# Optimization experiments

Hardware: AMD Instinct MI355X
Metric: run time of the kernel (lower is better)

Reference implementation:

```python
import jax, jax.numpy as jnp
import numpy as np

N, E = 50000, 800000          # nodes, directed edges
IN_DIM, HC, OUT_DIM = 128, 64, 128
NEG_SLOPE = 0.2               # PyG GATConv default leaky_relu slope
EPS = 1e-5                    # PyG LayerNorm default eps


def setup_inputs() -> dict:
    key = jax.random.key(0)
    ks = jax.random.split(key, 10)
    s = 0.1
    return {
        "x": jax.random.normal(ks[0], (N, IN_DIM), jnp.float32),
        "edge_index": jax.random.randint(ks[1], (2, E), 0, N, dtype=jnp.int32),
        # conv1: GATConv(IN_DIM -> HC, heads=2, concat=True)
        "W1": jax.random.normal(ks[2], (IN_DIM, 2 * HC), jnp.float32) * s,
        "att_src1": jax.random.normal(ks[3], (2, HC), jnp.float32) * s,
        "att_dst1": jax.random.normal(ks[4], (2, HC), jnp.float32) * s,
        "b1": jnp.zeros((2 * HC,), jnp.float32),
        "ln1_w": jnp.ones((2 * HC,), jnp.float32),
        "ln1_b": jnp.zeros((2 * HC,), jnp.float32),
        # conv2: GATConv(2*HC -> OUT_DIM, heads=1, concat=False)
        "W2": jax.random.normal(ks[5], (2 * HC, OUT_DIM), jnp.float32) * s,
        "att_src2": jax.random.normal(ks[6], (1, OUT_DIM), jnp.float32) * s,
        "att_dst2": jax.random.normal(ks[7], (1, OUT_DIM), jnp.float32) * s,
        "b2": jnp.zeros((OUT_DIM,), jnp.float32),
        "ln2_w": jnp.ones((OUT_DIM,), jnp.float32),
        "ln2_b": jnp.zeros((OUT_DIM,), jnp.float32),
    }


def gat_conv(x, src, dst, W, att_src, att_dst, bias, heads, C, concat):
    """PyG GATConv (shared lin for src/dst, self-loops already in src/dst)."""
    n = x.shape[0]
    h = (x @ W).reshape(n, heads, C)                       # [N,H,C]
    a_src = jnp.einsum('nhc,hc->nh', h, att_src)           # [N,H]
    a_dst = jnp.einsum('nhc,hc->nh', h, att_dst)           # [N,H]
    e = jax.nn.leaky_relu(a_src[src] + a_dst[dst], NEG_SLOPE)   # [E',H]
    # numerically-stable softmax over incoming edges of each dst node
    emax = jax.ops.segment_max(e, dst, num_segments=n)     # [N,H] (self-loops => non-empty)
    ex = jnp.exp(e - emax[dst])
    denom = jax.ops.segment_sum(ex, dst, num_segments=n)
    alpha = ex / (denom[dst] + 1e-16)                      # [E',H]
    out = jax.ops.segment_sum(h[src] * alpha[:, :, None], dst, num_segments=n)  # [N,H,C]
    out = out.reshape(n, heads * C) if concat else out.mean(axis=1)
    return out + bias


def graph_layernorm(x, w, b):
    """PyG LayerNorm, mode='graph', single graph: normalize over ALL nodes+features."""
    mean = x.mean()
    xc = x - mean
    var = (xc * xc).mean()
    return xc * jax.lax.rsqrt(var + EPS) * w + b


def reference(x, edge_index, W1, att_src1, att_dst1, b1, ln1_w, ln1_b,
              W2, att_src2, att_dst2, b2, ln2_w, ln2_b):
    n = x.shape[0]
    loop = jnp.arange(n, dtype=edge_index.dtype)
    src = jnp.concatenate([edge_index[0], loop])           # add self-loops for GAT convs
    dst = jnp.concatenate([edge_index[1], loop])

    h = gat_conv(x, src, dst, W1, att_src1, att_dst1, b1, heads=2, C=HC, concat=True)
    h = jax.nn.relu(graph_layernorm(h, ln1_w, ln1_b))
    h = gat_conv(h, src, dst, W2, att_src2, att_dst2, b2, heads=1, C=OUT_DIM, concat=False)
    h = graph_layernorm(h, ln2_w, ln2_b)

    # SimpleConv(aggr='mean') over the ORIGINAL edges (no self-loops), then residual
    s0, d0 = edge_index[0], edge_index[1]
    agg = jax.ops.segment_sum(h[s0], d0, num_segments=n)
    cnt = jax.ops.segment_sum(jnp.ones(s0.shape, h.dtype), d0, num_segments=n)
    mean_agg = agg / jnp.maximum(cnt, 1.0)[:, None]
    return jax.nn.relu(mean_agg + x)
```

## Files before the change

kernel.cpp:

```cpp
#include <hip/hip_runtime.h>
#include <hip/hip_bf16.h>
#include <cstdint>
#include <cstddef>

#define NN 50000
#define EE 800000
#define DD 128
#define NEG 0.2f
#define EPSL 1e-5f

#define NB   196
#define EPB  4096
#define NBKT 196
#define HM   (NBKT * NB)

#define GROWS 64
#define AB    (NN / 8)

typedef __hip_bfloat16 bf16;
typedef short short8 __attribute__((ext_vector_type(8)));
typedef float f32x4 __attribute__((ext_vector_type(4)));

__device__ inline float bflo(unsigned u) { return __uint_as_float(u << 16); }
__device__ inline float bfhi(unsigned u) { return __uint_as_float(u & 0xffff0000u); }
__device__ inline float bf2f(unsigned short u) { return __uint_as_float((unsigned)u << 16); }

__device__ inline unsigned short f2bf(float f) {
    __bf16 h = (__bf16)f;
    return __builtin_bit_cast(unsigned short, h);
}
__device__ inline unsigned pack2(float a, float b) {
    return (unsigned)f2bf(a) | ((unsigned)f2bf(b) << 16);
}

__device__ inline void store4(float* Out, size_t idx, float4 v) {
    *(float4*)&Out[idx] = v;
}
__device__ inline void store4(bf16* Out, size_t idx, float4 v) {
    union { bf16 b[4]; ushort4 u; } cv;
    cv.b[0] = (bf16)v.x; cv.b[1] = (bf16)v.y; cv.b[2] = (bf16)v.z; cv.b[3] = (bf16)v.w;
    *(ushort4*)&Out[idx] = cv.u;
}


__global__ __launch_bounds__(256) void hist_kernel(const int* __restrict__ ei,
                                                   int* __restrict__ histG) {
    __shared__ int lh[NBKT];
    int tid = threadIdx.x;
    for (int t = tid; t < NBKT; t += 256) lh[t] = 0;
    __syncthreads();
    int base = blockIdx.x * EPB;
    #pragma unroll
    for (int j = 0; j < EPB / 1024; ++j) {
        int i4 = base + (j * 256 + tid) * 4;
        if (i4 < EE) {
            int4 d4 = *(const int4*)&ei[EE + i4];
            atomicAdd(&lh[(unsigned)d4.x >> 8], 1);
            atomicAdd(&lh[(unsigned)d4.y >> 8], 1);
            atomicAdd(&lh[(unsigned)d4.z >> 8], 1);
            atomicAdd(&lh[(unsigned)d4.w >> 8], 1);
        }
    }
    __syncthreads();
    for (int t = tid; t < NBKT; t += 256) histG[t * NB + blockIdx.x] = lh[t];
}

__global__ __launch_bounds__(1024) void scan_hist_kernel(const int* __restrict__ histG,
                                                         int* __restrict__ offs,
                                                         int* __restrict__ bstart) {
    __shared__ int wsum[16];
    __shared__ int carry_s;
    int tid = threadIdx.x, lane = tid & 63, wv = tid >> 6;
    if (tid == 0) carry_s = 0;
    __syncthreads();
    for (int base = 0; base < HM; base += 4096) {
        int i4 = base + tid * 4;
        int4 v = make_int4(0, 0, 0, 0);
        if (i4 + 3 < HM) v = *(const int4*)&histG[i4];
        else {
            if (i4 + 0 < HM) v.x = histG[i4 + 0];
            if (i4 + 1 < HM) v.y = histG[i4 + 1];
            if (i4 + 2 < HM) v.z = histG[i4 + 2];
            if (i4 + 3 < HM) v.w = histG[i4 + 3];
        }
        int tsum = v.x + v.y + v.z + v.w;
        int x = tsum;
        for (int off = 1; off < 64; off <<= 1) {
            int t = __shfl_up(x, off);
            if (lane >= off) x += t;
        }
        if (lane == 63) wsum[wv] = x;
        __syncthreads();
        if (wv == 0) {
            int s = (lane < 16) ? wsum[lane] : 0;
            for (int off = 1; off < 16; off <<= 1) {
                int t = __shfl_up(s, off);
                if (lane >= off) s += t;
            }
            if (lane < 16) wsum[lane] = s;
        }
        __syncthreads();
        int waveoff = (wv == 0) ? 0 : wsum[wv - 1];
        int carry = carry_s;
        int o0 = carry + waveoff + x - tsum;
        int o1 = o0 + v.x, o2 = o1 + v.y, o3 = o2 + v.z;
        if (i4 + 3 < HM) *(int4*)&offs[i4] = make_int4(o0, o1, o2, o3);
        else {
            if (i4 + 0 < HM) offs[i4 + 0] = o0;
            if (i4 + 1 < HM) offs[i4 + 1] = o1;
            if (i4 + 2 < HM) offs[i4 + 2] = o2;
            if (i4 + 3 < HM) offs[i4 + 3] = o3;
        }
        if (i4 < HM && (i4 % NB) == 0) bstart[i4 / NB] = o0;
        __syncthreads();
        if (tid == 0) carry_s += wsum[15];
        __syncthreads();
    }
    if (tid == 0) bstart[NBKT] = carry_s;
}

__global__ __launch_bounds__(256) void scatter_pass1_kernel(const int* __restrict__ ei,
                                                            const int* __restrict__ offs,
                                                            unsigned* __restrict__ tmp) {
    __shared__ int lofs[NBKT];
    int tid = threadIdx.x;
    for (int t = tid; t < NBKT; t += 256) lofs[t] = offs[t * NB + blockIdx.x];
    __syncthreads();
    int base = blockIdx.x * EPB;
    #pragma unroll
    for (int j = 0; j < EPB / 1024; ++j) {
        int i4 = base + (j * 256 + tid) * 4;
        if (i4 < EE) {
            int4 s4 = *(const int4*)&ei[i4];
            int4 d4 = *(const int4*)&ei[EE + i4];
            unsigned k0 = ((unsigned)d4.x << 16) | (unsigned)s4.x;
            unsigned k1 = ((unsigned)d4.y << 16) | (unsigned)s4.y;
            unsigned k2 = ((unsigned)d4.z << 16) | (unsigned)s4.z;
            unsigned k3 = ((unsigned)d4.w << 16) | (unsigned)s4.w;
            tmp[atomicAdd(&lofs[(unsigned)d4.x >> 8], 1)] = k0;
            tmp[atomicAdd(&lofs[(unsigned)d4.y >> 8], 1)] = k1;
            tmp[atomicAdd(&lofs[(unsigned)d4.z >> 8], 1)] = k2;
            tmp[atomicAdd(&lofs[(unsigned)d4.w >> 8], 1)] = k3;
        }
    }
}

__global__ __launch_bounds__(256) void bucket_sort_kernel(const unsigned* __restrict__ tmp,
                                                          const int* __restrict__ bstart,
                                                          unsigned* __restrict__ col,
                                                          int* __restrict__ row_ptr) {
    __shared__ int cnt[256];
    __shared__ int cpos[256];
    __shared__ int wtot[4];
    int tid = threadIdx.x, lane = tid & 63, wv = tid >> 6;
    int s0 = bstart[blockIdx.x], s1 = bstart[blockIdx.x + 1];
    cnt[tid] = 0;
    __syncthreads();
    for (int i = s0 + tid; i < s1; i += 256)
        atomicAdd(&cnt[(tmp[i] >> 16) & 0xFF], 1);
    __syncthreads();
    int v = cnt[tid];
    int x = v;
    for (int off = 1; off < 64; off <<= 1) {
        int t = __shfl_up(x, off);
        if (lane >= off) x += t;
    }
    if (lane == 63) wtot[wv] = x;
    __syncthreads();
    int add = 0;
    for (int k = 0; k < wv; ++k) add += wtot[k];
    int start = s0 + add + x - v;
    cpos[tid] = start;
    int d = blockIdx.x * 256 + tid;
    if (d <= NN) row_ptr[d] = start;
    __syncthreads();
    for (int i = s0 + tid; i < s1; i += 256) {
        unsigned key = tmp[i];
        int pos = atomicAdd(&cpos[(key >> 16) & 0xFF], 1);
        col[pos] = key;
    }
}

template <int H, bool LN, typename XT>
__global__ __launch_bounds__(512) void gemm_attn(const XT* __restrict__ X,
                                                 const float* __restrict__ W,
                                                 const float* __restrict__ att_s,
                                                 const float* __restrict__ att_d,
                                                 const double* __restrict__ stats,
                                                 const float* __restrict__ lnw,
                                                 const float* __restrict__ lnb,
                                                 bf16* __restrict__ Hout,
                                                 float* __restrict__ a_src,
                                                 float* __restrict__ a_dst) {
    __shared__ __align__(16) char lds[(128 * 136 + 64 * 136) * 2 + 2048];
    unsigned short* Bt = (unsigned short*)lds;
    unsigned short* As = (unsigned short*)(lds + 128 * 136 * 2);
    float* Cs = (float*)lds;
    float* psum = (float*)(lds + (128 * 136 + 64 * 136) * 2);

    int tid = threadIdx.x;
    int row0 = blockIdx.x * GROWS;

    {
        int c = tid & 127, kg = tid >> 7;
        #pragma unroll 2
        for (int i = 0; i < 8; ++i) {
            int k0 = i * 16 + kg * 4;
            float wa = W[(size_t)(k0 + 0) * DD + c];
            float wb = W[(size_t)(k0 + 1) * DD + c];
            float wcv = W[(size_t)(k0 + 2) * DD + c];
            float wdv = W[(size_t)(k0 + 3) * DD + c];
            uint2 pk = make_uint2(pack2(wa, wb), pack2(wcv, wdv));
            *(uint2*)&Bt[c * 136 + k0] = pk;
        }
    }
    {
        int sub = tid & 31, rq = tid >> 5;
        int c4 = sub * 4;
        float mean = 0.f, inv = 1.f;
        float4 lw4 = make_float4(1.f, 1.f, 1.f, 1.f), lb4 = make_float4(0.f, 0.f, 0.f, 0.f);
        if (LN) {
            const double M = (double)NN * DD;
            double mean_d = stats[0] / M;
            double var_d = stats[1] / M - mean_d * mean_d;
            mean = (float)mean_d;
            inv = rsqrtf((float)var_d + EPSL);
            lw4 = *(const float4*)&lnw[c4];
            lb4 = *(const float4*)&lnb[c4];
        }
        #pragma unroll
        for (int i = 0; i < 4; ++i) {
            int r = i * 16 + rq;
            int row = row0 + r;
            float4 xv = make_float4(0.f, 0.f, 0.f, 0.f);
            if (row < NN) {
                if constexpr (sizeof(XT) == 4) {
                    xv = *(const float4*)&((const float*)X)[(size_t)row * DD + c4];
                } else {
                    ushort4 xb = *(const ushort4*)&((const unsigned short*)X)[(size_t)row * DD + c4];
                    xv = make_float4(bf2f(xb.x), bf2f(xb.y), bf2f(xb.z), bf2f(xb.w));
                }
            }
            if (LN) {
                xv.x = fmaxf((xv.x - mean) * inv * lw4.x + lb4.x, 0.f);
                xv.y = fmaxf((xv.y - mean) * inv * lw4.y + lb4.y, 0.f);
                xv.z = fmaxf((xv.z - mean) * inv * lw4.z + lb4.z, 0.f);
                xv.w = fmaxf((xv.w - mean) * inv * lw4.w + lb4.w, 0.f);
            }
            uint2 pk = make_uint2(pack2(xv.x, xv.y), pack2(xv.z, xv.w));
            *(uint2*)&As[r * 136 + c4] = pk;
        }
    }
    __syncthreads();

    int lane = tid & 63, w = tid >> 6;
    int rg = w & 3, cg = w >> 2;
    int l15 = lane & 15, quad = lane >> 4;
    f32x4 acc[4];
    #pragma unroll
    for (int t = 0; t < 4; ++t) acc[t] = 0.f;
    const unsigned short* Arow = As + (rg * 16 + l15) * 136 + quad * 8;
    const unsigned short* Brow = Bt + l15 * 136 + quad * 8;
    #pragma unroll
    for (int ks = 0; ks < 4; ++ks) {
        short8 a = *(const short8*)(Arow + ks * 32);
        #pragma unroll
        for (int tt = 0; tt < 4; ++tt) {
            short8 b = *(const short8*)(Brow + (cg * 4 + tt) * 16 * 136 + ks * 32);
            acc[tt] = __builtin_amdgcn_mfma_f32_16x16x32_bf16(a, b, acc[tt], 0, 0, 0);
        }
    }
    __syncthreads();

    #pragma unroll
    for (int tt = 0; tt < 4; ++tt)
        #pragma unroll
        for (int r = 0; r < 4; ++r)
            Cs[(rg * 16 + quad * 4 + r) * 132 + (cg * 4 + tt) * 16 + l15] = acc[tt][r];

    float ds[4] = {0.f, 0.f, 0.f, 0.f}, dd[4] = {0.f, 0.f, 0.f, 0.f};
    #pragma unroll
    for (int tt = 0; tt < 4; ++tt) {
        int cc = (cg * 4 + tt) * 16 + l15;
        float as_ = att_s[cc], ad_ = att_d[cc];
        #pragma unroll
        for (int r = 0; r < 4; ++r) {
            ds[r] = fmaf(acc[tt][r], as_, ds[r]);
            dd[r] = fmaf(acc[tt][r], ad_, dd[r]);
        }
    }
    #pragma unroll
    for (int off = 1; off < 16; off <<= 1) {
        #pragma unroll
        for (int r = 0; r < 4; ++r) {
            ds[r] += __shfl_xor(ds[r], off);
            dd[r] += __shfl_xor(dd[r], off);
        }
    }
    if (l15 == 0) {
        #pragma unroll
        for (int r = 0; r < 4; ++r) {
            int rr = rg * 16 + quad * 4 + r;
            int row = row0 + rr;
            if (H == 2) {
                if (row < NN) {
                    a_src[row * 2 + cg] = ds[r];
                    a_dst[row * 2 + cg] = dd[r];
                }
            } else {
                psum[cg * 64 + rr] = ds[r];
                psum[128 + cg * 64 + rr] = dd[r];
            }
        }
    }
    __syncthreads();

    if (H == 1 && tid < 64) {
        int row = row0 + tid;
        if (row < NN) {
            a_src[row] = psum[tid] + psum[64 + tid];
            a_dst[row] = psum[128 + tid] + psum[192 + tid];
        }
    }

    {
        int sub = tid & 31, rq = tid >> 5;
        int c4 = sub * 4;
        unsigned short* Hp = (unsigned short*)Hout;
        #pragma unroll
        for (int i = 0; i < 4; ++i) {
            int r = i * 16 + rq;
            int row = row0 + r;
            if (row < NN) {
                float4 cv = *(const float4*)&Cs[r * 132 + c4];
                ushort4 pk;
                pk.x = f2bf(cv.x); pk.y = f2bf(cv.y);
                pk.z = f2bf(cv.z); pk.w = f2bf(cv.w);
                *(ushort4*)&Hp[(size_t)row * DD + c4] = pk;
            }
        }
    }
}

template <int H, typename OT>
__global__ __launch_bounds__(256) void gat_agg(const int* __restrict__ row_ptr,
                                               const unsigned* __restrict__ col,
                                               const bf16* __restrict__ Hin,
                                               const float* __restrict__ a_src,
                                               const float* __restrict__ a_dst,
                                               const float* __restrict__ bias,
                                               OT* __restrict__ Out,
                                               float2* __restrict__ pstats) {
    int tid = threadIdx.x;
    int sl = tid & 31;
    int hw = tid >> 5;
    int n = blockIdx.x * 8 + hw;
    int c0 = sl * 4;
    const int head4 = (H == 2) ? (sl >> 4) : 0;

    int beg = row_ptr[n], end = row_ptr[n + 1];
    int deg = end - beg;

    float ad0 = a_dst[n * H + 0];
    float ad1 = (H == 2) ? a_dst[n * H + 1] : 0.f;
    const ushort* Hp = (const ushort*)Hin + c0;

    float acc[4] = {0.f, 0.f, 0.f, 0.f};
    float dl0 = 0.f, dl1 = 0.f;

    for (int base = 0; base < deg; base += 32) {
        int ecnt = min(32, deg - base);
        int sv = 0; float w0v = 0.f, w1v = 0.f;
        if (sl < ecnt) {
            sv = (int)(col[beg + base + sl] & 0xffffu);
            if (H == 2) {
                float2 av = *(const float2*)&a_src[sv * 2];
                float e0 = av.x + ad0; e0 = (e0 > 0.f) ? e0 : NEG * e0;
                float e1 = av.y + ad1; e1 = (e1 > 0.f) ? e1 : NEG * e1;
                w0v = __expf(e0); w1v = __expf(e1);
                dl0 += w0v; dl1 += w1v;
            } else {
                float e0 = a_src[sv] + ad0; e0 = (e0 > 0.f) ? e0 : NEG * e0;
                w0v = __expf(e0);
                dl0 += w0v;
            }
        }
        int j = 0;
        for (; j + 7 < ecnt; j += 8) {
            int s[8]; float ww[8];
            uint2 h[8];
            #pragma unroll
            for (int u = 0; u < 8; ++u) {
                s[u] = __shfl(sv, j + u, 32);
                if (H == 2) {
                    float a0 = __shfl(w0v, j + u, 32), b0 = __shfl(w1v, j + u, 32);
                    ww[u] = head4 ? b0 : a0;
                } else {
                    ww[u] = __shfl(w0v, j + u, 32);
                }
            }
            #pragma unroll
            for (int u = 0; u < 8; ++u) h[u] = *(const uint2*)(Hp + (size_t)s[u] * DD);
            #pragma unroll
            for (int u = 0; u < 8; ++u) {
                acc[0] = fmaf(ww[u], bflo(h[u].x), acc[0]);
                acc[1] = fmaf(ww[u], bfhi(h[u].x), acc[1]);
                acc[2] = fmaf(ww[u], bflo(h[u].y), acc[2]);
                acc[3] = fmaf(ww[u], bfhi(h[u].y), acc[3]);
            }
        }
        for (; j < ecnt; ++j) {
            int s = __shfl(sv, j, 32);
            float w;
            if (H == 2) {
                float a0 = __shfl(w0v, j, 32), b0 = __shfl(w1v, j, 32);
                w = head4 ? b0 : a0;
            } else {
                w = __shfl(w0v, j, 32);
            }
            uint2 hv = *(const uint2*)(Hp + (size_t)s * DD);
            acc[0] = fmaf(w, bflo(hv.x), acc[0]); acc[1] = fmaf(w, bfhi(hv.x), acc[1]);
            acc[2] = fmaf(w, bflo(hv.y), acc[2]); acc[3] = fmaf(w, bfhi(hv.y), acc[3]);
        }
    }

    #pragma unroll
    for (int off = 1; off < 32; off <<= 1) {
        dl0 += __shfl_xor(dl0, off);
        if (H == 2) dl1 += __shfl_xor(dl1, off);
    }

    float e0 = a_src[n * H + 0] + ad0; e0 = (e0 > 0.f) ? e0 : NEG * e0;
    float ws0 = __expf(e0);
    float ws1 = 0.f;
    if (H == 2) {
        float e1 = a_src[n * H + 1] + ad1; e1 = (e1 > 0.f) ? e1 : NEG * e1;
        ws1 = __expf(e1);
    }
    float den = (H == 2 && head4) ? (dl1 + ws1) : (dl0 + ws0);
    float wself = (H == 2 && head4) ? ws1 : ws0;
    float rinv = 1.f / (den + 1e-16f);
    uint2 hs = *(const uint2*)(Hp + (size_t)n * DD);
    float4 bi = *(const float4*)&bias[c0];
    float4 o;
    o.x = fmaf(wself, bflo(hs.x), acc[0]) * rinv + bi.x;
    o.y = fmaf(wself, bfhi(hs.x), acc[1]) * rinv + bi.y;
    o.z = fmaf(wself, bflo(hs.y), acc[2]) * rinv + bi.z;
    o.w = fmaf(wself, bfhi(hs.y), acc[3]) * rinv + bi.w;
    store4(Out, (size_t)n * DD + c0, o);

    float t1 = o.x + o.y + o.z + o.w;
    float t2 = o.x * o.x + o.y * o.y + o.z * o.z + o.w * o.w;
    #pragma unroll
    for (int off = 1; off < 32; off <<= 1) {
        t1 += __shfl_xor(t1, off);
        t2 += __shfl_xor(t2, off);
    }
    __shared__ float2 ps[8];
    if (sl == 0) ps[hw] = make_float2(t1, t2);
    __syncthreads();
    if (tid == 0) {
        float a = 0.f, b = 0.f;
        #pragma unroll
        for (int k = 0; k < 8; ++k) { a += ps[k].x; b += ps[k].y; }
        pstats[blockIdx.x] = make_float2(a, b);
    }
}

__global__ __launch_bounds__(1024) void reduce_stats_kernel(const float2* __restrict__ pstats,
                                                            double* __restrict__ stats) {
    int tid = threadIdx.x, lane = tid & 63, wv = tid >> 6;
    double s1 = 0.0, s2 = 0.0;
    for (int i = tid; i < AB; i += 1024) {
        float2 v = pstats[i];
        s1 += (double)v.x; s2 += (double)v.y;
    }
    for (int off = 32; off; off >>= 1) {
        s1 += __shfl_xor(s1, off);
        s2 += __shfl_xor(s2, off);
    }
    __shared__ double w1[16], w2[16];
    if (lane == 0) { w1[wv] = s1; w2[wv] = s2; }
    __syncthreads();
    if (tid == 0) {
        double a = 0.0, b = 0.0;
        for (int i = 0; i < 16; ++i) { a += w1[i]; b += w2[i]; }
        stats[0] = a; stats[1] = b;
    }
}

__global__ __launch_bounds__(256) void simpleconv_kernel(const int* __restrict__ row_ptr,
                                                         const unsigned* __restrict__ col,
                                                         const bf16* __restrict__ Hin,
                                                         const float* __restrict__ X,
                                                         const double* __restrict__ stats,
                                                         const float* __restrict__ lnw,
                                                         const float* __restrict__ lnb,
                                                         float* __restrict__ Out) {
    int tid = threadIdx.x;
    int sl = tid & 31;
    int n = blockIdx.x * 8 + (tid >> 5);
    int c0 = sl * 4;
    int beg = row_ptr[n], end = row_ptr[n + 1];
    int deg = end - beg;
    const ushort* Hp = (const ushort*)Hin + c0;

    float acc[4] = {0.f, 0.f, 0.f, 0.f};
    for (int base = 0; base < deg; base += 32) {
        int ecnt = min(32, deg - base);
        int sv = 0;
        if (sl < ecnt) sv = (int)(col[beg + base + sl] & 0xffffu);
        int j = 0;
        for (; j + 7 < ecnt; j += 8) {
            int s[8]; uint2 h[8];
            #pragma unroll
            for (int u = 0; u < 8; ++u) s[u] = __shfl(sv, j + u, 32);
            #pragma unroll
            for (int u = 0; u < 8; ++u) h[u] = *(const uint2*)(Hp + (size_t)s[u] * DD);
            #pragma unroll
            for (int u = 0; u < 8; ++u) {
                acc[0] += bflo(h[u].x); acc[1] += bfhi(h[u].x);
                acc[2] += bflo(h[u].y); acc[3] += bfhi(h[u].y);
            }
        }
        for (; j < ecnt; ++j) {
            int s = __shfl(sv, j, 32);
            uint2 hv = *(const uint2*)(Hp + (size_t)s * DD);
            acc[0] += bflo(hv.x); acc[1] += bfhi(hv.x);
            acc[2] += bflo(hv.y); acc[3] += bfhi(hv.y);
        }
    }

    const double M = (double)NN * DD;
    double mean_d = stats[0] / M;
    double var_d = stats[1] / M - mean_d * mean_d;
    float mean2 = (float)mean_d;
    float inv2 = rsqrtf((float)var_d + EPSL);
    float rc = 1.f / (float)((deg > 0) ? deg : 1);
    float4 xr = *(const float4*)&X[(size_t)n * DD + c0];
    float4 o;
    if (deg > 0) {
        float4 lw = *(const float4*)&lnw[c0];
        float4 lb = *(const float4*)&lnb[c0];
        o.x = (acc[0] * rc - mean2) * inv2 * lw.x + lb.x;
        o.y = (acc[1] * rc - mean2) * inv2 * lw.y + lb.y;
        o.z = (acc[2] * rc - mean2) * inv2 * lw.z + lb.z;
        o.w = (acc[3] * rc - mean2) * inv2 * lw.w + lb.w;
    } else {
        o.x = o.y = o.z = o.w = 0.f;
    }
    o.x = fmaxf(o.x + xr.x, 0.f);
    o.y = fmaxf(o.y + xr.y, 0.f);
    o.z = fmaxf(o.z + xr.z, 0.f);
    o.w = fmaxf(o.w + xr.w, 0.f);
    *(float4*)&Out[(size_t)n * DD + c0] = o;
}

extern "C" void kernel_launch(void* const* d_in, const int* in_sizes, int n_in,
                              void* d_out, int out_size, void* d_ws, size_t ws_size,
                              hipStream_t stream) {
    const float* x    = (const float*)d_in[0];
    const int*   ei   = (const int*)d_in[1];
    const float* W1   = (const float*)d_in[2];
    const float* as1  = (const float*)d_in[3];
    const float* ad1  = (const float*)d_in[4];
    const float* b1   = (const float*)d_in[5];
    const float* ln1w = (const float*)d_in[6];
    const float* ln1b = (const float*)d_in[7];
    const float* W2   = (const float*)d_in[8];
    const float* as2  = (const float*)d_in[9];
    const float* ad2  = (const float*)d_in[10];
    const float* b2   = (const float*)d_in[11];
    const float* ln2w = (const float*)d_in[12];
    const float* ln2b = (const float*)d_in[13];
    float* out = (float*)d_out;

    char* p = (char*)d_ws;
    auto alloc = [&](size_t bytes) {
        void* r = (void*)p;
        p += (bytes + 255) & ~(size_t)255;
        return r;
    };
    unsigned* tmp     = (unsigned*)alloc((size_t)EE * 4);
    unsigned* col     = (unsigned*)alloc((size_t)EE * 4);
    int*      histG   = (int*)alloc((size_t)HM * 4);
    int*      offs    = (int*)alloc((size_t)HM * 4);
    int*      bstart  = (int*)alloc((size_t)(NBKT + 1) * 4);
    int*      row_ptr = (int*)alloc((size_t)(NN + 256) * 4);
    double*   stats1  = (double*)alloc(16);
    double*   stats2  = (double*)alloc(16);
    float2*   pstats  = (float2*)alloc((size_t)AB * 8);
    bf16*     bufA    = (bf16*)alloc((size_t)NN * DD * 2);
    bf16*     bufB    = (bf16*)alloc((size_t)NN * DD * 2);
    float*    aS1     = (float*)alloc((size_t)NN * 2 * 4);
    float*    aD1     = (float*)alloc((size_t)NN * 2 * 4);
    float*    aS2     = (float*)alloc((size_t)NN * 4);
    float*    aD2     = (float*)alloc((size_t)NN * 4);

    hist_kernel<<<NB, 256, 0, stream>>>(ei, histG);
    scan_hist_kernel<<<1, 1024, 0, stream>>>(histG, offs, bstart);
    scatter_pass1_kernel<<<NB, 256, 0, stream>>>(ei, offs, tmp);
    bucket_sort_kernel<<<NBKT, 256, 0, stream>>>(tmp, bstart, col, row_ptr);

    const int GB = (NN + GROWS - 1) / GROWS;

    gemm_attn<2, false, float><<<GB, 512, 0, stream>>>(x, W1, as1, ad1,
                                                       nullptr, nullptr, nullptr,
                                                       bufA, aS1, aD1);
    gat_agg<2, bf16><<<AB, 256, 0, stream>>>(row_ptr, col, bufA, aS1, aD1, b1, bufB, pstats);
    reduce_stats_kernel<<<1, 1024, 0, stream>>>(pstats, stats1);

    gemm_attn<1, true, bf16><<<GB, 512, 0, stream>>>(bufB, W2, as2, ad2,
                                                     stats1, ln1w, ln1b,
                                                     bufA, aS2, aD2);
    gat_agg<1, bf16><<<AB, 256, 0, stream>>>(row_ptr, col, bufA, aS2, aD2, b2, bufB, pstats);
    reduce_stats_kernel<<<1, 1024, 0, stream>>>(pstats, stats2);

    simpleconv_kernel<<<AB, 256, 0, stream>>>(row_ptr, col, bufB, x,
                                              stats2, ln2w, ln2b, out);
}
```

Before: 272.9 us.

## Fuse edge scatter with first GEMM and fold stats reduction into aggregation

Merges the edge scatter pass and the layer-1 GEMM/attention kernel into one launch, with the leading blocks doing the scatter and the rest doing the GEMM, so the two independent jobs run concurrently. It also removes the two single-block reduce_stats launches by having the last-finishing gat_agg block, detected through an atomic counter and thread fences, reduce the partial statistics. This cuts launch count and idle gaps. The cost is that the scatter blocks now share the GEMM kernel's large LDS footprint, and that counters must be reset every call, which scan_hist does.

```diff
diff --git a/kernel.cpp b/kernel.cpp
--- a/kernel.cpp
+++ b/kernel.cpp
@@ -67,11 +67,12 @@
 
 __global__ __launch_bounds__(1024) void scan_hist_kernel(const int* __restrict__ histG,
                                                          int* __restrict__ offs,
-                                                         int* __restrict__ bstart) {
+                                                         int* __restrict__ bstart,
+                                                         int* __restrict__ counters) {
     __shared__ int wsum[16];
     __shared__ int carry_s;
     int tid = threadIdx.x, lane = tid & 63, wv = tid >> 6;
-    if (tid == 0) carry_s = 0;
+    if (tid == 0) { carry_s = 0; counters[0] = 0; counters[1] = 0; }
     __syncthreads();
     for (int base = 0; base < HM; base += 4096) {
         int i4 = base + tid * 4;
@@ -119,32 +120,6 @@
     if (tid == 0) bstart[NBKT] = carry_s;
 }
 
-__global__ __launch_bounds__(256) void scatter_pass1_kernel(const int* __restrict__ ei,
-                                                            const int* __restrict__ offs,
-                                                            unsigned* __restrict__ tmp) {
-    __shared__ int lofs[NBKT];
-    int tid = threadIdx.x;
-    for (int t = tid; t < NBKT; t += 256) lofs[t] = offs[t * NB + blockIdx.x];
-    __syncthreads();
-    int base = blockIdx.x * EPB;
-    #pragma unroll
-    for (int j = 0; j < EPB / 1024; ++j) {
-        int i4 = base + (j * 256 + tid) * 4;
-        if (i4 < EE) {
-            int4 s4 = *(const int4*)&ei[i4];
-            int4 d4 = *(const int4*)&ei[EE + i4];
-            unsigned k0 = ((unsigned)d4.x << 16) | (unsigned)s4.x;
-            unsigned k1 = ((unsigned)d4.y << 16) | (unsigned)s4.y;
-            unsigned k2 = ((unsigned)d4.z << 16) | (unsigned)s4.z;
-            unsigned k3 = ((unsigned)d4.w << 16) | (unsigned)s4.w;
-            tmp[atomicAdd(&lofs[(unsigned)d4.x >> 8], 1)] = k0;
-            tmp[atomicAdd(&lofs[(unsigned)d4.y >> 8], 1)] = k1;
-            tmp[atomicAdd(&lofs[(unsigned)d4.z >> 8], 1)] = k2;
-            tmp[atomicAdd(&lofs[(unsigned)d4.w >> 8], 1)] = k3;
-        }
-    }
-}
-
 __global__ __launch_bounds__(256) void bucket_sort_kernel(const unsigned* __restrict__ tmp,
                                                           const int* __restrict__ bstart,
                                                           unsigned* __restrict__ col,
@@ -182,16 +157,17 @@
 }
 
 template <int H, bool LN, typename XT>
-__global__ __launch_bounds__(512) void gemm_attn(const XT* __restrict__ X,
-                                                 const float* __restrict__ W,
-                                                 const float* __restrict__ att_s,
-                                                 const float* __restrict__ att_d,
-                                                 const double* __restrict__ stats,
-                                                 const float* __restrict__ lnw,
-                                                 const float* __restrict__ lnb,
-                                                 bf16* __restrict__ Hout,
-                                                 float* __restrict__ a_src,
-                                                 float* __restrict__ a_dst) {
+__device__ __forceinline__ void gemm_attn_body(int gb,
+                                               const XT* __restrict__ X,
+                                               const float* __restrict__ W,
+                                               const float* __restrict__ att_s,
+                                               const float* __restrict__ att_d,
+                                               const double* __restrict__ stats,
+                                               const float* __restrict__ lnw,
+                                               const float* __restrict__ lnb,
+                                               bf16* __restrict__ Hout,
+                                               float* __restrict__ a_src,
+                                               float* __restrict__ a_dst) {
     __shared__ __align__(16) char lds[(128 * 136 + 64 * 136) * 2 + 2048];
     unsigned short* Bt = (unsigned short*)lds;
     unsigned short* As = (unsigned short*)(lds + 128 * 136 * 2);
@@ -199,7 +175,7 @@
     float* psum = (float*)(lds + (128 * 136 + 64 * 136) * 2);
 
     int tid = threadIdx.x;
-    int row0 = blockIdx.x * GROWS;
+    int row0 = gb * GROWS;
 
     {
         int c = tid & 127, kg = tid >> 7;
@@ -342,6 +318,59 @@
     }
 }
 
+template <int H, bool LN, typename XT>
+__global__ __launch_bounds__(512) void gemm_attn(const XT* __restrict__ X,
+                                                 const float* __restrict__ W,
+                                                 const float* __restrict__ att_s,
+                                                 const float* __restrict__ att_d,
+                                                 const double* __restrict__ stats,
+                                                 const float* __restrict__ lnw,
+                                                 const float* __restrict__ lnb,
+                                                 bf16* __restrict__ Hout,
+                                                 float* __restrict__ a_src,
+                                                 float* __restrict__ a_dst) {
+    gemm_attn_body<H, LN, XT>(blockIdx.x, X, W, att_s, att_d, stats, lnw, lnb,
+                              Hout, a_src, a_dst);
+}
+
+__global__ __launch_bounds__(512) void scatter_gemm1(const int* __restrict__ ei,
+                                                     const int* __restrict__ offs,
+                                                     unsigned* __restrict__ tmp,
+                                                     const float* __restrict__ X,
+                                                     const float* __restrict__ W,
+                                                     const float* __restrict__ att_s,
+                                                     const float* __restrict__ att_d,
+                                                     bf16* __restrict__ Hout,
+                                                     float* __restrict__ a_src,
+                                                     float* __restrict__ a_dst) {
+    if (blockIdx.x < NB) {
+        __shared__ int lofs[NBKT];
+        int tid = threadIdx.x;
+        for (int t = tid; t < NBKT; t += 512) lofs[t] = offs[t * NB + blockIdx.x];
+        __syncthreads();
+        int base = blockIdx.x * EPB;
+        #pragma unroll
+        for (int j = 0; j < EPB / 2048; ++j) {
+            int i4 = base + (j * 512 + tid) * 4;
+            if (i4 < EE) {
+                int4 s4 = *(const int4*)&ei[i4];
+                int4 d4 = *(const int4*)&ei[EE + i4];
+                unsigned k0 = ((unsigned)d4.x << 16) | (unsigned)s4.x;
+                unsigned k1 = ((unsigned)d4.y << 16) | (unsigned)s4.y;
+                unsigned k2 = ((unsigned)d4.z << 16) | (unsigned)s4.z;
+                unsigned k3 = ((unsigned)d4.w << 16) | (unsigned)s4.w;
+                tmp[atomicAdd(&lofs[(unsigned)d4.x >> 8], 1)] = k0;
+                tmp[atomicAdd(&lofs[(unsigned)d4.y >> 8], 1)] = k1;
+                tmp[atomicAdd(&lofs[(unsigned)d4.z >> 8], 1)] = k2;
+                tmp[atomicAdd(&lofs[(unsigned)d4.w >> 8], 1)] = k3;
+            }
+        }
+    } else {
+        gemm_attn_body<2, false, float>(blockIdx.x - NB, X, W, att_s, att_d,
+                                        nullptr, nullptr, nullptr, Hout, a_src, a_dst);
+    }
+}
+
 template <int H, typename OT>
 __global__ __launch_bounds__(256) void gat_agg(const int* __restrict__ row_ptr,
                                                const unsigned* __restrict__ col,
@@ -350,7 +379,9 @@
                                                const float* __restrict__ a_dst,
                                                const float* __restrict__ bias,
                                                OT* __restrict__ Out,
-                                               float2* __restrict__ pstats) {
+                                               float2* __restrict__ pstats,
+                                               int* __restrict__ counter,
+                                               double* __restrict__ stats) {
     int tid = threadIdx.x;
     int sl = tid & 31;
     int hw = tid >> 5;
@@ -457,6 +488,7 @@
         t2 += __shfl_xor(t2, off);
     }
     __shared__ float2 ps[8];
+    __shared__ int lastFlag;
     if (sl == 0) ps[hw] = make_float2(t1, t2);
     __syncthreads();
     if (tid == 0) {
@@ -464,28 +496,32 @@
         #pragma unroll
         for (int k = 0; k < 8; ++k) { a += ps[k].x; b += ps[k].y; }
         pstats[blockIdx.x] = make_float2(a, b);
-    }
-}
-
-__global__ __launch_bounds__(1024) void reduce_stats_kernel(const float2* __restrict__ pstats,
-                                                            double* __restrict__ stats) {
-    int tid = threadIdx.x, lane = tid & 63, wv = tid >> 6;
-    double s1 = 0.0, s2 = 0.0;
-    for (int i = tid; i < AB; i += 1024) {
-        float2 v = pstats[i];
-        s1 += (double)v.x; s2 += (double)v.y;
-    }
-    for (int off = 32; off; off >>= 1) {
-        s1 += __shfl_xor(s1, off);
-        s2 += __shfl_xor(s2, off);
-    }
-    __shared__ double w1[16], w2[16];
-    if (lane == 0) { w1[wv] = s1; w2[wv] = s2; }
-    __syncthreads();
-    if (tid == 0) {
-        double a = 0.0, b = 0.0;
-        for (int i = 0; i < 16; ++i) { a += w1[i]; b += w2[i]; }
-        stats[0] = a; stats[1] = b;
+        __threadfence();
+        int old = atomicAdd(counter, 1);
+        lastFlag = (old == AB - 1) ? 1 : 0;
+    }
+    __syncthreads();
+    if (lastFlag) {
+        __threadfence();
+        int lane = tid & 63, wv = tid >> 6;
+        double s1 = 0.0, s2 = 0.0;
+        for (int i = tid; i < AB; i += 256) {
+            float2 v = pstats[i];
+            s1 += (double)v.x; s2 += (double)v.y;
+        }
+        for (int off = 32; off; off >>= 1) {
+            s1 += __shfl_xor(s1, off);
+            s2 += __shfl_xor(s2, off);
+        }
+        __shared__ double w1[4], w2[4];
+        if (lane == 0) { w1[wv] = s1; w2[wv] = s2; }
+        __syncthreads();
+        if (tid == 0) {
+            double a = 0.0, b = 0.0;
+            #pragma unroll
+            for (int i = 0; i < 4; ++i) { a += w1[i]; b += w2[i]; }
+            stats[0] = a; stats[1] = b;
+        }
     }
 }
 
@@ -590,6 +626,7 @@
     double*   stats1  = (double*)alloc(16);
     double*   stats2  = (double*)alloc(16);
     float2*   pstats  = (float2*)alloc((size_t)AB * 8);
+    int*      counters= (int*)alloc(16);
     bf16*     bufA    = (bf16*)alloc((size_t)NN * DD * 2);
     bf16*     bufB    = (bf16*)alloc((size_t)NN * DD * 2);
     float*    aS1     = (float*)alloc((size_t)NN * 2 * 4);
@@ -597,24 +634,22 @@
     float*    aS2     = (float*)alloc((size_t)NN * 4);
     float*    aD2     = (float*)alloc((size_t)NN * 4);
 
+    const int GB = (NN + GROWS - 1) / GROWS;
+
     hist_kernel<<<NB, 256, 0, stream>>>(ei, histG);
-    scan_hist_kernel<<<1, 1024, 0, stream>>>(histG, offs, bstart);
-    scatter_pass1_kernel<<<NB, 256, 0, stream>>>(ei, offs, tmp);
+    scan_hist_kernel<<<1, 1024, 0, stream>>>(histG, offs, bstart, counters);
+    scatter_gemm1<<<NB + GB, 512, 0, stream>>>(ei, offs, tmp,
+                                               x, W1, as1, ad1, bufA, aS1, aD1);
     bucket_sort_kernel<<<NBKT, 256, 0, stream>>>(tmp, bstart, col, row_ptr);
 
-    const int GB = (NN + GROWS - 1) / GROWS;
-
-    gemm_attn<2, false, float><<<GB, 512, 0, stream>>>(x, W1, as1, ad1,
-                                                       nullptr, nullptr, nullptr,
-                                                       bufA, aS1, aD1);
-    gat_agg<2, bf16><<<AB, 256, 0, stream>>>(row_ptr, col, bufA, aS1, aD1, b1, bufB, pstats);
-    reduce_stats_kernel<<<1, 1024, 0, stream>>>(pstats, stats1);
+    gat_agg<2, bf16><<<AB, 256, 0, stream>>>(row_ptr, col, bufA, aS1, aD1, b1, bufB,
+                                             pstats, counters + 0, stats1);
 
     gemm_attn<1, true, bf16><<<GB, 512, 0, stream>>>(bufB, W2, as2, ad2,
                                                      stats1, ln1w, ln1b,
                                                      bufA, aS2, aD2);
-    gat_agg<1, bf16><<<AB, 256, 0, stream>>>(row_ptr, col, bufA, aS2, aD2, b2, bufB, pstats);
-    reduce_stats_kernel<<<1, 1024, 0, stream>>>(pstats, stats2);
+    gat_agg<1, bf16><<<AB, 256, 0, stream>>>(row_ptr, col, bufA, aS2, aD2, b2, bufB,
+                                             pstats, counters + 1, stats2);
 
     simpleconv_kernel<<<AB, 256, 0, stream>>>(row_ptr, col, bufB, x,
                                               stats2, ln2w, ln2b, out);
```

After: 623.3 us. +128.3%, slower.
